# Kernel tuning notes

Measured on AMD Instinct MI355X. Metric: run time of the kernel, lower is better.

## Reference

```python
import jax, jax.numpy as jnp
import numpy as np

D_MODEL = 1024
N_HEADS = 16
D_K = D_MODEL // N_HEADS
ROPE_THETA = 10000.0


def setup_inputs() -> dict:
    key = jax.random.key(0)
    ks = jax.random.split(key, 5)
    B, S = 2, 2048
    std = (2.0 / (D_MODEL + D_MODEL)) ** 0.5
    x = jax.random.normal(ks[0], (B, S, D_MODEL), dtype=jnp.float32)
    Wq = jax.random.normal(ks[1], (D_MODEL, D_MODEL), dtype=jnp.float32) * std
    Wk = jax.random.normal(ks[2], (D_MODEL, D_MODEL), dtype=jnp.float32) * std
    Wv = jax.random.normal(ks[3], (D_MODEL, D_MODEL), dtype=jnp.float32) * std
    Wo = jax.random.normal(ks[4], (D_MODEL, D_MODEL), dtype=jnp.float32) * std
    token_positions = jnp.arange(S, dtype=jnp.int64 if jax.config.jax_enable_x64 else jnp.int32)
    return {"x": x, "Wq": Wq, "Wk": Wk, "Wv": Wv, "Wo": Wo,
            "token_positions": token_positions}


def _apply_rope(t, token_positions):
    # t: [B, H, S, d_k]; token_positions: [S]
    inv_freq = 1.0 / (ROPE_THETA ** (jnp.arange(0, D_K, 2, dtype=jnp.float32) / D_K))  # [d_k/2]
    freqs = token_positions.astype(jnp.float32)[:, None] * inv_freq[None, :]  # [S, d_k/2]
    cos, sin = jnp.cos(freqs), jnp.sin(freqs)
    x1, x2 = t[..., ::2], t[..., 1::2]
    xr = x1 * cos - x2 * sin
    yr = x1 * sin + x2 * cos
    # interleave back to even/odd positions
    out = jnp.stack([xr, yr], axis=-1).reshape(t.shape)
    return out


def reference(x, Wq, Wk, Wv, Wo, token_positions):
    B, S, D = x.shape
    H, dk = N_HEADS, D_K
    # projections: weight is [d_out, d_in], applied as x @ W.T
    def proj_heads(W):
        y = jnp.einsum('bsd,ed->bse', x, W)
        return y.reshape(B, S, H, dk).transpose(0, 2, 1, 3)  # [B,H,S,dk]
    q = proj_heads(Wq)
    k = proj_heads(Wk)
    v = proj_heads(Wv)
    q = _apply_rope(q, token_positions)
    k = _apply_rope(k, token_positions)
    scores = jnp.einsum('bhqd,bhkd->bhqk', q, k) / jnp.sqrt(jnp.float32(dk))
    causal = jnp.tril(jnp.ones((S, S), dtype=bool))
    scores = jnp.where(causal, scores, -jnp.inf)
    attn = jax.nn.softmax(scores, axis=-1)
    out = jnp.einsum('bhqk,bhkd->bhqd', attn, v)  # [B,H,S,dk]
    out = out.transpose(0, 2, 1, 3).reshape(B, S, D)
    return jnp.einsum('bsd,ed->bse', out, Wo)
```

## Files before the change

### kernel.cpp

```cpp
#include <hip/hip_runtime.h>

typedef __bf16 bf16x8 __attribute__((ext_vector_type(8)));
typedef float f32x4 __attribute__((ext_vector_type(4)));
typedef unsigned short u16x8 __attribute__((ext_vector_type(8)));


__device__ __forceinline__ unsigned short f2bf(float f) {
  unsigned u = __builtin_bit_cast(unsigned, f);
  u = (u + 0x7FFFu + ((u >> 16) & 1u)) >> 16;
  return (unsigned short)u;
}

__device__ __forceinline__ unsigned cvt_pk_bf16(float lo, float hi) {
  unsigned r;
  asm("v_cvt_pk_bf16_f32 %0, %1, %2" : "=v"(r) : "v"(lo), "v"(hi));
  return r;
}

__device__ __forceinline__ void load_lds16(const void* g, void* l) {
  __builtin_amdgcn_global_load_lds(
      (__attribute__((address_space(1))) void*)g,
      (__attribute__((address_space(3))) void*)l, 16, 0, 0);
}

__global__ __launch_bounds__(256) void k_convert(
    const float* __restrict__ x,
    const float* __restrict__ wq, const float* __restrict__ wk,
    const float* __restrict__ wv, const float* __restrict__ wo,
    unsigned short* __restrict__ xb,
    unsigned short* __restrict__ wqb, unsigned short* __restrict__ wkb,
    unsigned short* __restrict__ wvb, unsigned short* __restrict__ wob) {
  const int g = blockIdx.x * 256 + threadIdx.x;
  const float* src;
  unsigned short* dst;
  int off;
  if (g < (1 << 20)) {
    src = x; dst = xb; off = g;
  } else {
    const int q = g - (1 << 20);
    const int t = q >> 18;
    off = q & ((1 << 18) - 1);
    src = (t == 0) ? wq : (t == 1) ? wk : (t == 2) ? wv : wo;
    dst = (t == 0) ? wqb : (t == 1) ? wkb : (t == 2) ? wvb : wob;
  }
  const float4 v = ((const float4*)src)[off];
  ushort4 r;
  r.x = f2bf(v.x); r.y = f2bf(v.y); r.z = f2bf(v.z); r.w = f2bf(v.w);
  ((ushort4*)dst)[off] = r;
}

__global__ __launch_bounds__(256) void k_rope_tab(const int* __restrict__ tpos,
                                                  float* __restrict__ ct,
                                                  float* __restrict__ st) {
  const int idx = blockIdx.x * 256 + threadIdx.x;
  const int s = idx >> 5, i = idx & 31;
  const double p = (double)tpos[s];
  const double f = p * pow(10000.0, -(double)(2 * i) / 64.0);
  ct[idx] = (float)cos(f);
  st[idx] = (float)sin(f);
}

__device__ __forceinline__ void gemm_core_1024(
    const unsigned short* __restrict__ Ag,
    const unsigned short* __restrict__ Bg,
    unsigned short* As, unsigned short* Bs, f32x4 (&acc)[4][4], int tid) {
  const int lane = tid & 63;
  const int w = tid >> 6;
  const int wm = (w >> 1) * 64;
  const int wn = (w & 1) * 64;
  const int lr = lane & 15;
  const int lg8 = (lane >> 4) * 8;
  const int c0 = tid, c1 = 256 + tid;
  const int ar0 = c0 >> 2, ac0 = (c0 & 3) * 8;
  const int ar1 = c1 >> 2, ac1 = (c1 & 3) * 8;

  auto stage = [&](int buf, int kt) {
    unsigned short* Ab = As + buf * 4096;
    unsigned short* Bb = Bs + buf * 4096;
    load_lds16(Ag + ar0 * 1024 + kt + ac0, Ab + c0 * 8);
    load_lds16(Ag + ar1 * 1024 + kt + ac1, Ab + c1 * 8);
    load_lds16(Bg + ar0 * 1024 + kt + ac0, Bb + c0 * 8);
    load_lds16(Bg + ar1 * 1024 + kt + ac1, Bb + c1 * 8);
  };

  stage(0, 0);
  stage(1, 32);
  int cur = 0;
  for (int ki = 0; ki < 32; ++ki) {
    if (ki + 2 < 32) {
      int nb = cur + 2; if (nb >= 3) nb -= 3;
      stage(nb, (ki + 2) * 32);
      asm volatile("s_waitcnt vmcnt(8)" ::: "memory");
    } else if (ki + 1 < 32) {
      asm volatile("s_waitcnt vmcnt(4)" ::: "memory");
    } else {
      asm volatile("s_waitcnt vmcnt(0)" ::: "memory");
    }
    __builtin_amdgcn_s_barrier();
    const unsigned short* Ab = As + cur * 4096;
    const unsigned short* Bb = Bs + cur * 4096;
    bf16x8 af[4], bfv[4];
#pragma unroll
    for (int mi = 0; mi < 4; ++mi)
      af[mi] = *(const bf16x8*)(Ab + (wm + mi * 16 + lr) * 32 + lg8);
#pragma unroll
    for (int ni = 0; ni < 4; ++ni)
      bfv[ni] = *(const bf16x8*)(Bb + (wn + ni * 16 + lr) * 32 + lg8);
    __builtin_amdgcn_s_setprio(1);
#pragma unroll
    for (int mi = 0; mi < 4; ++mi)
#pragma unroll
      for (int ni = 0; ni < 4; ++ni)
        acc[mi][ni] = __builtin_amdgcn_mfma_f32_16x16x32_bf16(
            af[mi], bfv[ni], acc[mi][ni], 0, 0, 0);
    __builtin_amdgcn_s_setprio(0);
    __builtin_amdgcn_s_barrier();
    ++cur; if (cur == 3) cur = 0;
  }
}

__global__ __launch_bounds__(256) void k_proj(
    const unsigned short* __restrict__ Xb,
    const unsigned short* __restrict__ Wq, const unsigned short* __restrict__ Wk,
    const unsigned short* __restrict__ Wv,
    const float* __restrict__ ctab, const float* __restrict__ stab,
    unsigned short* __restrict__ Qo, unsigned short* __restrict__ Ko,
    unsigned short* __restrict__ Vo) {
  __shared__ __align__(16) unsigned short As[3 * 128 * 32];
  __shared__ __align__(16) unsigned short Bs[3 * 128 * 32];
  const int z = blockIdx.z;
  const unsigned short* Wsel = (z == 0) ? Wq : (z == 1) ? Wk : Wv;
  unsigned short* Out = (z == 0) ? Qo : (z == 1) ? Ko : Vo;
  const int tid = threadIdx.x;
  const int bm = blockIdx.x * 128, bn = blockIdx.y * 128;
  f32x4 acc[4][4] = {};
  gemm_core_1024(Xb + (size_t)bm * 1024, Wsel + (size_t)bn * 1024, As, Bs, acc, tid);

  const int lane = tid & 63, w = tid >> 6;
  const int wm = (w >> 1) * 64, wn = (w & 1) * 64;
  const int lr = lane & 15, lg = lane >> 4;

  if (z == 2) {
#pragma unroll
    for (int mi = 0; mi < 4; ++mi) {
      const int r0 = bm + wm + mi * 16 + lg * 4;
      const int s = r0 & 2047, b = r0 >> 11;
#pragma unroll
      for (int ni = 0; ni < 4; ++ni) {
        const int e = bn + wn + ni * 16 + lr;
        const int h = e >> 6, d = e & 63;
        ushort4 pk;
        pk.x = f2bf(acc[mi][ni][0]);
        pk.y = f2bf(acc[mi][ni][1]);
        pk.z = f2bf(acc[mi][ni][2]);
        pk.w = f2bf(acc[mi][ni][3]);
        *(ushort4*)&Out[((size_t)(b * 16 + h) * 64 + d) * 2048 + s] = pk;
      }
    }
    return;
  }

  const bool odd = lane & 1;
#pragma unroll
  for (int mi = 0; mi < 4; ++mi) {
#pragma unroll
    for (int ni = 0; ni < 4; ++ni) {
#pragma unroll
      for (int reg = 0; reg < 4; ++reg) {
        const int r = bm + wm + mi * 16 + lg * 4 + reg;
        const int e = bn + wn + ni * 16 + lr;
        float val = acc[mi][ni][reg];
        const float partner = __shfl_xor(val, 1);
        const int s = r & 2047, b = r >> 11;
        const int h = e >> 6, d = e & 63;
        const int i = d >> 1;
        const float c = ctab[s * 32 + i];
        const float sn = stab[s * 32 + i];
        const float outv = odd ? (val * c + partner * sn) : (val * c - partner * sn);
        Out[((size_t)(b * 16 + h) * 2048 + s) * 64 + d] = f2bf(outv);
      }
    }
  }
}

__global__ __launch_bounds__(64, 2) void k_attn(
    const unsigned short* __restrict__ Q, const unsigned short* __restrict__ K,
    const unsigned short* __restrict__ Vt, unsigned short* __restrict__ O) {
  __shared__ __align__(16) unsigned short Vs[2][64 * 64];
  __shared__ __align__(16) unsigned short Pl[16 * 68];
  const int L = blockIdx.x;
  const int bh = (L & 7) * 4 + ((L >> 3) & 3);
  const int p = L >> 5;
  const int qrowA = p * 16, qrowB = (127 - p) * 16;
  const int Ta = (qrowA + 79) >> 6;
  const int Tb = (qrowB + 79) >> 6;
  const int lane = threadIdx.x & 63;
  const int lr = lane & 15, lg = lane >> 4;
  const unsigned short* Qg = Q + (size_t)bh * 2048 * 64;
  const unsigned short* Kg = K + (size_t)bh * 2048 * 64;
  const unsigned short* Vg = Vt + (size_t)bh * 64 * 2048;

  bf16x8 qfA[2], qfB[2];
#pragma unroll
  for (int h = 0; h < 2; ++h) {
    qfA[h] = *(const bf16x8*)(Qg + (qrowA + lr) * 64 + h * 32 + lg * 8);
    qfB[h] = *(const bf16x8*)(Qg + (qrowB + lr) * 64 + h * 32 + lg * 8);
  }

  f32x4 oA[4] = {}, oB[4] = {};
  float mA = -__builtin_inff(), lA = 0.f;
  float mB = -__builtin_inff(), lB = 0.f;

  const float SCL = 0.125f * 1.44269504088896f;

  const int kbase = lr * 64 + lg * 8;
  const int vbase = (lane >> 3) * 2048 + (((lane & 7) ^ (lane >> 3)) * 8);

  auto loadK = [&](bf16x8 (&kd)[4][2], int kv) {
    const unsigned short* base = Kg + (size_t)kv * 4096 + kbase;
#pragma unroll
    for (int nt = 0; nt < 4; ++nt)
#pragma unroll
      for (int h = 0; h < 2; ++h)
        kd[nt][h] = *(const bf16x8*)(base + nt * 1024 + h * 32);
  };
  auto issueV = [&](int buf, int kv) {
    const unsigned short* src = Vg + kv * 64 + vbase;
    unsigned short* dst = &Vs[buf][0] + lane * 8;
#pragma unroll
    for (int i0 = 0; i0 < 8; ++i0)
      load_lds16(src + i0 * 16384, dst + i0 * 512);
  };

  auto process = [&](f32x4 (&s)[4], float& m, float& l, f32x4 (&oacc)[4],
                     int qrow, bool needmask, int kv) {
    if (needmask) {
      const int qg = qrow + lr;
#pragma unroll
      for (int nt = 0; nt < 4; ++nt)
#pragma unroll
        for (int reg = 0; reg < 4; ++reg) {
          const int kg = kv * 64 + nt * 16 + lg * 4 + reg;
          if (kg > qg) s[nt][reg] = -__builtin_inff();
        }
    }
    float t0 = fmaxf(fmaxf(s[0][0], s[0][1]), fmaxf(s[0][2], s[0][3]));
    float t1 = fmaxf(fmaxf(s[1][0], s[1][1]), fmaxf(s[1][2], s[1][3]));
    float t2 = fmaxf(fmaxf(s[2][0], s[2][1]), fmaxf(s[2][2], s[2][3]));
    float t3 = fmaxf(fmaxf(s[3][0], s[3][1]), fmaxf(s[3][2], s[3][3]));
    float pm = fmaxf(fmaxf(t0, t1), fmaxf(t2, t3));
    pm = fmaxf(pm, __shfl_xor(pm, 16));
    pm = fmaxf(pm, __shfl_xor(pm, 32));
    if (__any(pm > m)) {
      const float mn = fmaxf(m, pm);
      const float al = exp2f(SCL * (m - mn));
      m = mn;
      l *= al;
#pragma unroll
      for (int nt = 0; nt < 4; ++nt)
#pragma unroll
        for (int reg = 0; reg < 4; ++reg) oacc[nt][reg] *= al;
    }
    const float msc = SCL * m;
    float rs = 0.f;
    unsigned short* prow = Pl + lr * 68;
#pragma unroll
    for (int nt = 0; nt < 4; ++nt) {
      const float p0 = exp2f(s[nt][0] * SCL - msc);
      const float p1 = exp2f(s[nt][1] * SCL - msc);
      const float p2 = exp2f(s[nt][2] * SCL - msc);
      const float p3 = exp2f(s[nt][3] * SCL - msc);
      rs += (p0 + p1) + (p2 + p3);
      const unsigned w01 = cvt_pk_bf16(p0, p1);
      const unsigned w23 = cvt_pk_bf16(p2, p3);
      ushort4 pk;
      pk.x = (unsigned short)w01; pk.y = (unsigned short)(w01 >> 16);
      pk.z = (unsigned short)w23; pk.w = (unsigned short)(w23 >> 16);
      *(ushort4*)(prow + nt * 16 + lg * 4) = pk;
    }
    rs += __shfl_xor(rs, 16);
    rs += __shfl_xor(rs, 32);
    l += rs;
  };

  bf16x8 kbufA[4][2], kbufB[4][2];
  loadK(kbufA, 0);
  issueV(0, 0);

  auto iter = [&](int t, bf16x8 (&kc)[4][2], bf16x8 (&kn)[4][2]) {
    const bool more = (t + 1 < Tb);
    const bool actA = (t < Ta);
    asm volatile("s_waitcnt lgkmcnt(0)" ::: "memory");
    if (more) { loadK(kn, t + 1); issueV((t + 1) & 1, t + 1); }

    f32x4 sB[4], sA[4];
    __builtin_amdgcn_s_setprio(1);
#pragma unroll
    for (int nt = 0; nt < 4; ++nt) {
      f32x4 z = {0.f, 0.f, 0.f, 0.f};
      z = __builtin_amdgcn_mfma_f32_16x16x32_bf16(kc[nt][0], qfB[0], z, 0, 0, 0);
      sB[nt] = __builtin_amdgcn_mfma_f32_16x16x32_bf16(kc[nt][1], qfB[1], z, 0, 0, 0);
    }
    if (actA)
#pragma unroll
      for (int nt = 0; nt < 4; ++nt) {
        f32x4 z = {0.f, 0.f, 0.f, 0.f};
        z = __builtin_amdgcn_mfma_f32_16x16x32_bf16(kc[nt][0], qfA[0], z, 0, 0, 0);
        sA[nt] = __builtin_amdgcn_mfma_f32_16x16x32_bf16(kc[nt][1], qfA[1], z, 0, 0, 0);
      }
    __builtin_amdgcn_s_setprio(0);

    process(sB, mB, lB, oB, qrowB, t == Tb - 1, t);
    bf16x8 paB[2], paA[2];
#pragma unroll
    for (int ks = 0; ks < 2; ++ks)
      paB[ks] = *(const bf16x8*)(Pl + lr * 68 + ks * 32 + lg * 8);
    if (actA) {
      process(sA, mA, lA, oA, qrowA, t == Ta - 1, t);
#pragma unroll
      for (int ks = 0; ks < 2; ++ks)
        paA[ks] = *(const bf16x8*)(Pl + lr * 68 + ks * 32 + lg * 8);
    }

    if (more) asm volatile("s_waitcnt vmcnt(16)" ::: "memory");
    else      asm volatile("s_waitcnt vmcnt(0)" ::: "memory");

    const unsigned short* Vw = &Vs[t & 1][0];
    __builtin_amdgcn_s_setprio(1);
#pragma unroll
    for (int nt = 0; nt < 4; ++nt) {
      const int row = nt * 16 + lr;
      const bf16x8 vb0 = *(const bf16x8*)(Vw + row * 64 + ((lg ^ (row & 7)) * 8));
      const bf16x8 vb1 = *(const bf16x8*)(Vw + row * 64 + (((lg + 4) ^ (row & 7)) * 8));
      oB[nt] = __builtin_amdgcn_mfma_f32_16x16x32_bf16(vb0, paB[0], oB[nt], 0, 0, 0);
      oB[nt] = __builtin_amdgcn_mfma_f32_16x16x32_bf16(vb1, paB[1], oB[nt], 0, 0, 0);
      if (actA) {
        oA[nt] = __builtin_amdgcn_mfma_f32_16x16x32_bf16(vb0, paA[0], oA[nt], 0, 0, 0);
        oA[nt] = __builtin_amdgcn_mfma_f32_16x16x32_bf16(vb1, paA[1], oA[nt], 0, 0, 0);
      }
    }
    __builtin_amdgcn_s_setprio(0);
  };

  int t = 0;
  for (;;) {
    iter(t, kbufA, kbufB); ++t; if (t >= Tb) break;
    iter(t, kbufB, kbufA); ++t; if (t >= Tb) break;
  }

  const int b = bh >> 4, h = bh & 15;
  auto wrO = [&](f32x4 (&oacc)[4], float l, int qrow) {
    const float inv = 1.0f / l;
    unsigned short* dst = &O[((size_t)b * 2048 + qrow + lr) * 1024 + h * 64];
#pragma unroll
    for (int nt = 0; nt < 4; ++nt) {
      const unsigned w01 = cvt_pk_bf16(oacc[nt][0] * inv, oacc[nt][1] * inv);
      const unsigned w23 = cvt_pk_bf16(oacc[nt][2] * inv, oacc[nt][3] * inv);
      ushort4 pk;
      pk.x = (unsigned short)w01; pk.y = (unsigned short)(w01 >> 16);
      pk.z = (unsigned short)w23; pk.w = (unsigned short)(w23 >> 16);
      *(ushort4*)(dst + nt * 16 + lg * 4) = pk;
    }
  };
  wrO(oA, lA, qrowA);
  wrO(oB, lB, qrowB);
}

__global__ __launch_bounds__(256) void k_out(const unsigned short* __restrict__ Ab,
                                             const unsigned short* __restrict__ Wo,
                                             float* __restrict__ Out) {
  __shared__ __align__(16) unsigned short As[3 * 128 * 32];
  __shared__ __align__(16) unsigned short Bs[3 * 128 * 32];
  const int tid = threadIdx.x;
  const int bm = blockIdx.x * 128, bn = blockIdx.y * 128;
  f32x4 acc[4][4] = {};
  gemm_core_1024(Ab + (size_t)bm * 1024, Wo + (size_t)bn * 1024, As, Bs, acc, tid);
  const int lane = tid & 63, w = tid >> 6;
  const int wm = (w >> 1) * 64, wn = (w & 1) * 64;
  const int lr = lane & 15, lg = lane >> 4;
#pragma unroll
  for (int mi = 0; mi < 4; ++mi)
#pragma unroll
    for (int ni = 0; ni < 4; ++ni)
#pragma unroll
      for (int reg = 0; reg < 4; ++reg) {
        const int r = bm + wm + mi * 16 + lg * 4 + reg;
        const int e = bn + wn + ni * 16 + lr;
        Out[(size_t)r * 1024 + e] = acc[mi][ni][reg];
      }
}

extern "C" void kernel_launch(void* const* d_in, const int* in_sizes, int n_in,
                              void* d_out, int out_size, void* d_ws, size_t ws_size,
                              hipStream_t stream) {
  const float* x = (const float*)d_in[0];
  const float* Wq = (const float*)d_in[1];
  const float* Wk = (const float*)d_in[2];
  const float* Wv = (const float*)d_in[3];
  const float* Wo = (const float*)d_in[4];
  const int* tpos = (const int*)d_in[5];
  float* out = (float*)d_out;
  char* ws = (char*)d_ws;
  const size_t MB = 1024 * 1024;
  unsigned short* xb = (unsigned short*)(ws);
  unsigned short* wqb = (unsigned short*)(ws + 8 * MB);
  unsigned short* wkb = (unsigned short*)(ws + 10 * MB);
  unsigned short* wvb = (unsigned short*)(ws + 12 * MB);
  unsigned short* wob = (unsigned short*)(ws + 14 * MB);
  unsigned short* Qb = (unsigned short*)(ws + 16 * MB);
  unsigned short* Kb = (unsigned short*)(ws + 24 * MB);
  unsigned short* Vtb = (unsigned short*)(ws + 32 * MB);
  unsigned short* Ab = (unsigned short*)(ws + 40 * MB);
  float* ctab = (float*)(ws + 48 * MB);
  float* stab = (float*)(ws + 48 * MB + 256 * 1024);

  k_convert<<<dim3(8192), dim3(256), 0, stream>>>(x, Wq, Wk, Wv, Wo, xb, wqb, wkb,
                                                  wvb, wob);
  k_rope_tab<<<dim3(256), dim3(256), 0, stream>>>(tpos, ctab, stab);
  k_proj<<<dim3(32, 8, 3), dim3(256), 0, stream>>>(xb, wqb, wkb, wvb, ctab, stab,
                                                   Qb, Kb, Vtb);
  k_attn<<<dim3(2048), dim3(64), 0, stream>>>(Qb, Kb, Vtb, Ab);
  k_out<<<dim3(32, 8), dim3(256), 0, stream>>>(Ab, wob, out);
}
```

Measured before the change: 156.2 us.

## Load V fragments directly to registers, compute softmax row sums by MFMA, shrink out-proj tile

The attention kernel drops the LDS staging of V and instead double-buffers V fragments in registers straight from global memory, along with K. It gives each query group its own P buffer in LDS. Softmax row sums are now computed with an MFMA against a ones vector instead of shuffle reductions. The output projection switches to 64-row tiles so it launches twice as many blocks. The changes aim to cut LDS traffic, waits and shuffles, and to improve occupancy, at the cost of more VGPRs and less coalesced V loads.

New measurement: 205.9 us. 1.32x slower.

```diff
diff --git a/kernel.cpp b/kernel.cpp
--- a/kernel.cpp
+++ b/kernel.cpp
@@ -119,6 +119,63 @@
   }
 }
 
+__device__ __forceinline__ void gemm_core_bm64(
+    const unsigned short* __restrict__ Ag,
+    const unsigned short* __restrict__ Bg,
+    unsigned short* As, unsigned short* Bs, f32x4 (&acc)[2][4], int tid) {
+  const int lane = tid & 63;
+  const int w = tid >> 6;
+  const int wm = (w >> 1) * 32;
+  const int wn = (w & 1) * 64;
+  const int lr = lane & 15;
+  const int lg8 = (lane >> 4) * 8;
+  const int ar = tid >> 2, ac = (tid & 3) * 8;
+  const int c0 = tid, c1 = 256 + tid;
+  const int br0 = c0 >> 2, bc0 = (c0 & 3) * 8;
+  const int br1 = c1 >> 2, bc1 = (c1 & 3) * 8;
+
+  auto stage = [&](int buf, int kt) {
+    load_lds16(Ag + ar * 1024 + kt + ac, As + buf * 2048 + tid * 8);
+    load_lds16(Bg + br0 * 1024 + kt + bc0, Bs + buf * 4096 + c0 * 8);
+    load_lds16(Bg + br1 * 1024 + kt + bc1, Bs + buf * 4096 + c1 * 8);
+  };
+
+  stage(0, 0);
+  stage(1, 32);
+  int cur = 0;
+  for (int ki = 0; ki < 32; ++ki) {
+    if (ki + 2 < 32) {
+      int nb = cur + 2; if (nb >= 3) nb -= 3;
+      stage(nb, (ki + 2) * 32);
+      asm volatile("s_waitcnt vmcnt(6)" ::: "memory");
+    } else if (ki + 1 < 32) {
+      asm volatile("s_waitcnt vmcnt(3)" ::: "memory");
+    } else {
+      asm volatile("s_waitcnt vmcnt(0)" ::: "memory");
+    }
+    __builtin_amdgcn_s_barrier();
+    const unsigned short* Ab = As + cur * 2048;
+    const unsigned short* Bb = Bs + cur * 4096;
+    bf16x8 af[2], bfv[4];
+#pragma unroll
+    for (int mi = 0; mi < 2; ++mi)
+      af[mi] = *(const bf16x8*)(Ab + (wm + mi * 16 + lr) * 32 + lg8);
+#pragma unroll
+    for (int ni = 0; ni < 4; ++ni)
+      bfv[ni] = *(const bf16x8*)(Bb + (wn + ni * 16 + lr) * 32 + lg8);
+    __builtin_amdgcn_s_setprio(1);
+#pragma unroll
+    for (int mi = 0; mi < 2; ++mi)
+#pragma unroll
+      for (int ni = 0; ni < 4; ++ni)
+        acc[mi][ni] = __builtin_amdgcn_mfma_f32_16x16x32_bf16(
+            af[mi], bfv[ni], acc[mi][ni], 0, 0, 0);
+    __builtin_amdgcn_s_setprio(0);
+    __builtin_amdgcn_s_barrier();
+    ++cur; if (cur == 3) cur = 0;
+  }
+}
+
 __global__ __launch_bounds__(256) void k_proj(
     const unsigned short* __restrict__ Xb,
     const unsigned short* __restrict__ Wq, const unsigned short* __restrict__ Wk,
@@ -186,8 +243,8 @@
 __global__ __launch_bounds__(64, 2) void k_attn(
     const unsigned short* __restrict__ Q, const unsigned short* __restrict__ K,
     const unsigned short* __restrict__ Vt, unsigned short* __restrict__ O) {
-  __shared__ __align__(16) unsigned short Vs[2][64 * 64];
-  __shared__ __align__(16) unsigned short Pl[16 * 68];
+  __shared__ __align__(16) unsigned short PlB[16 * 68];
+  __shared__ __align__(16) unsigned short PlA[16 * 68];
   const int L = blockIdx.x;
   const int bh = (L & 7) * 4 + ((L >> 3) & 3);
   const int p = L >> 5;
@@ -207,14 +264,19 @@
     qfB[h] = *(const bf16x8*)(Qg + (qrowB + lr) * 64 + h * 32 + lg * 8);
   }
 
+  u16x8 ouv;
+#pragma unroll
+  for (int j = 0; j < 8; ++j) ouv[j] = 0x3F80;
+  const bf16x8 onesf = __builtin_bit_cast(bf16x8, ouv);
+
   f32x4 oA[4] = {}, oB[4] = {};
-  float mA = -__builtin_inff(), lA = 0.f;
-  float mB = -__builtin_inff(), lB = 0.f;
+  f32x4 lAa = {}, lBa = {};
+  float mA = -__builtin_inff(), mB = -__builtin_inff();
 
   const float SCL = 0.125f * 1.44269504088896f;
 
   const int kbase = lr * 64 + lg * 8;
-  const int vbase = (lane >> 3) * 2048 + (((lane & 7) ^ (lane >> 3)) * 8);
+  const int vbase = lr * 2048 + lg * 8;
 
   auto loadK = [&](bf16x8 (&kd)[4][2], int kv) {
     const unsigned short* base = Kg + (size_t)kv * 4096 + kbase;
@@ -224,16 +286,17 @@
       for (int h = 0; h < 2; ++h)
         kd[nt][h] = *(const bf16x8*)(base + nt * 1024 + h * 32);
   };
-  auto issueV = [&](int buf, int kv) {
-    const unsigned short* src = Vg + kv * 64 + vbase;
-    unsigned short* dst = &Vs[buf][0] + lane * 8;
-#pragma unroll
-    for (int i0 = 0; i0 < 8; ++i0)
-      load_lds16(src + i0 * 16384, dst + i0 * 512);
-  };
-
-  auto process = [&](f32x4 (&s)[4], float& m, float& l, f32x4 (&oacc)[4],
-                     int qrow, bool needmask, int kv) {
+  auto loadV = [&](bf16x8 (&vd)[4][2], int kv) {
+    const unsigned short* base = Vg + vbase + kv * 64;
+#pragma unroll
+    for (int nt = 0; nt < 4; ++nt)
+#pragma unroll
+      for (int ks = 0; ks < 2; ++ks)
+        vd[nt][ks] = *(const bf16x8*)(base + nt * 16 * 2048 + ks * 32);
+  };
+
+  auto soft = [&](f32x4 (&s)[4], float& m, f32x4& la, f32x4 (&oacc)[4],
+                  int qrow, bool needmask, int kv, unsigned short* Pl) {
     if (needmask) {
       const int qg = qrow + lr;
 #pragma unroll
@@ -255,14 +318,14 @@
       const float mn = fmaxf(m, pm);
       const float al = exp2f(SCL * (m - mn));
       m = mn;
-      l *= al;
+#pragma unroll
+      for (int reg = 0; reg < 4; ++reg) la[reg] *= al;
 #pragma unroll
       for (int nt = 0; nt < 4; ++nt)
 #pragma unroll
         for (int reg = 0; reg < 4; ++reg) oacc[nt][reg] *= al;
     }
     const float msc = SCL * m;
-    float rs = 0.f;
     unsigned short* prow = Pl + lr * 68;
 #pragma unroll
     for (int nt = 0; nt < 4; ++nt) {
@@ -270,7 +333,6 @@
       const float p1 = exp2f(s[nt][1] * SCL - msc);
       const float p2 = exp2f(s[nt][2] * SCL - msc);
       const float p3 = exp2f(s[nt][3] * SCL - msc);
-      rs += (p0 + p1) + (p2 + p3);
       const unsigned w01 = cvt_pk_bf16(p0, p1);
       const unsigned w23 = cvt_pk_bf16(p2, p3);
       ushort4 pk;
@@ -278,20 +340,17 @@
       pk.z = (unsigned short)w23; pk.w = (unsigned short)(w23 >> 16);
       *(ushort4*)(prow + nt * 16 + lg * 4) = pk;
     }
-    rs += __shfl_xor(rs, 16);
-    rs += __shfl_xor(rs, 32);
-    l += rs;
-  };
-
-  bf16x8 kbufA[4][2], kbufB[4][2];
+  };
+
+  bf16x8 kbufA[4][2], kbufB[4][2], vbufA[4][2], vbufB[4][2];
   loadK(kbufA, 0);
-  issueV(0, 0);
-
-  auto iter = [&](int t, bf16x8 (&kc)[4][2], bf16x8 (&kn)[4][2]) {
+  loadV(vbufA, 0);
+
+  auto iter = [&](int t, bf16x8 (&kc)[4][2], bf16x8 (&kn)[4][2],
+                  bf16x8 (&vc)[4][2], bf16x8 (&vn)[4][2]) {
     const bool more = (t + 1 < Tb);
     const bool actA = (t < Ta);
-    asm volatile("s_waitcnt lgkmcnt(0)" ::: "memory");
-    if (more) { loadK(kn, t + 1); issueV((t + 1) & 1, t + 1); }
+    if (more) { loadK(kn, t + 1); loadV(vn, t + 1); }
 
     f32x4 sB[4], sA[4];
     __builtin_amdgcn_s_setprio(1);
@@ -310,33 +369,36 @@
       }
     __builtin_amdgcn_s_setprio(0);
 
-    process(sB, mB, lB, oB, qrowB, t == Tb - 1, t);
     bf16x8 paB[2], paA[2];
-#pragma unroll
-    for (int ks = 0; ks < 2; ++ks)
-      paB[ks] = *(const bf16x8*)(Pl + lr * 68 + ks * 32 + lg * 8);
     if (actA) {
-      process(sA, mA, lA, oA, qrowA, t == Ta - 1, t);
+      soft(sB, mB, lBa, oB, qrowB, t == Tb - 1, t, PlB);
+      soft(sA, mA, lAa, oA, qrowA, t == Ta - 1, t, PlA);
+#pragma unroll
+      for (int ks = 0; ks < 2; ++ks) {
+        paB[ks] = *(const bf16x8*)(PlB + lr * 68 + ks * 32 + lg * 8);
+        paA[ks] = *(const bf16x8*)(PlA + lr * 68 + ks * 32 + lg * 8);
+      }
+    } else {
+      soft(sB, mB, lBa, oB, qrowB, t == Tb - 1, t, PlB);
 #pragma unroll
       for (int ks = 0; ks < 2; ++ks)
-        paA[ks] = *(const bf16x8*)(Pl + lr * 68 + ks * 32 + lg * 8);
-    }
-
-    if (more) asm volatile("s_waitcnt vmcnt(16)" ::: "memory");
-    else      asm volatile("s_waitcnt vmcnt(0)" ::: "memory");
-
-    const unsigned short* Vw = &Vs[t & 1][0];
+        paB[ks] = *(const bf16x8*)(PlB + lr * 68 + ks * 32 + lg * 8);
+    }
+
     __builtin_amdgcn_s_setprio(1);
+    lBa = __builtin_amdgcn_mfma_f32_16x16x32_bf16(onesf, paB[0], lBa, 0, 0, 0);
+    lBa = __builtin_amdgcn_mfma_f32_16x16x32_bf16(onesf, paB[1], lBa, 0, 0, 0);
+    if (actA) {
+      lAa = __builtin_amdgcn_mfma_f32_16x16x32_bf16(onesf, paA[0], lAa, 0, 0, 0);
+      lAa = __builtin_amdgcn_mfma_f32_16x16x32_bf16(onesf, paA[1], lAa, 0, 0, 0);
+    }
 #pragma unroll
     for (int nt = 0; nt < 4; ++nt) {
-      const int row = nt * 16 + lr;
-      const bf16x8 vb0 = *(const bf16x8*)(Vw + row * 64 + ((lg ^ (row & 7)) * 8));
-      const bf16x8 vb1 = *(const bf16x8*)(Vw + row * 64 + (((lg + 4) ^ (row & 7)) * 8));
-      oB[nt] = __builtin_amdgcn_mfma_f32_16x16x32_bf16(vb0, paB[0], oB[nt], 0, 0, 0);
-      oB[nt] = __builtin_amdgcn_mfma_f32_16x16x32_bf16(vb1, paB[1], oB[nt], 0, 0, 0);
+      oB[nt] = __builtin_amdgcn_mfma_f32_16x16x32_bf16(vc[nt][0], paB[0], oB[nt], 0, 0, 0);
+      oB[nt] = __builtin_amdgcn_mfma_f32_16x16x32_bf16(vc[nt][1], paB[1], oB[nt], 0, 0, 0);
       if (actA) {
-        oA[nt] = __builtin_amdgcn_mfma_f32_16x16x32_bf16(vb0, paA[0], oA[nt], 0, 0, 0);
-        oA[nt] = __builtin_amdgcn_mfma_f32_16x16x32_bf16(vb1, paA[1], oA[nt], 0, 0, 0);
+        oA[nt] = __builtin_amdgcn_mfma_f32_16x16x32_bf16(vc[nt][0], paA[0], oA[nt], 0, 0, 0);
+        oA[nt] = __builtin_amdgcn_mfma_f32_16x16x32_bf16(vc[nt][1], paA[1], oA[nt], 0, 0, 0);
       }
     }
     __builtin_amdgcn_s_setprio(0);
@@ -344,8 +406,8 @@
 
   int t = 0;
   for (;;) {
-    iter(t, kbufA, kbufB); ++t; if (t >= Tb) break;
-    iter(t, kbufB, kbufA); ++t; if (t >= Tb) break;
+    iter(t, kbufA, kbufB, vbufA, vbufB); ++t; if (t >= Tb) break;
+    iter(t, kbufB, kbufA, vbufB, vbufA); ++t; if (t >= Tb) break;
   }
 
   const int b = bh >> 4, h = bh & 15;
@@ -362,24 +424,24 @@
       *(ushort4*)(dst + nt * 16 + lg * 4) = pk;
     }
   };
-  wrO(oA, lA, qrowA);
-  wrO(oB, lB, qrowB);
+  wrO(oA, lAa[0], qrowA);
+  wrO(oB, lBa[0], qrowB);
 }
 
 __global__ __launch_bounds__(256) void k_out(const unsigned short* __restrict__ Ab,
                                              const unsigned short* __restrict__ Wo,
                                              float* __restrict__ Out) {
-  __shared__ __align__(16) unsigned short As[3 * 128 * 32];
+  __shared__ __align__(16) unsigned short As[3 * 64 * 32];
   __shared__ __align__(16) unsigned short Bs[3 * 128 * 32];
   const int tid = threadIdx.x;
-  const int bm = blockIdx.x * 128, bn = blockIdx.y * 128;
-  f32x4 acc[4][4] = {};
-  gemm_core_1024(Ab + (size_t)bm * 1024, Wo + (size_t)bn * 1024, As, Bs, acc, tid);
+  const int bm = blockIdx.x * 64, bn = blockIdx.y * 128;
+  f32x4 acc[2][4] = {};
+  gemm_core_bm64(Ab + (size_t)bm * 1024, Wo + (size_t)bn * 1024, As, Bs, acc, tid);
   const int lane = tid & 63, w = tid >> 6;
-  const int wm = (w >> 1) * 64, wn = (w & 1) * 64;
+  const int wm = (w >> 1) * 32, wn = (w & 1) * 64;
   const int lr = lane & 15, lg = lane >> 4;
 #pragma unroll
-  for (int mi = 0; mi < 4; ++mi)
+  for (int mi = 0; mi < 2; ++mi)
 #pragma unroll
     for (int ni = 0; ni < 4; ++ni)
 #pragma unroll
@@ -420,5 +482,5 @@
   k_proj<<<dim3(32, 8, 3), dim3(256), 0, stream>>>(xb, wqb, wkb, wvb, ctab, stab,
                                                    Qb, Kb, Vtb);
   k_attn<<<dim3(2048), dim3(64), 0, stream>>>(Qb, Kb, Vtb, Ab);
-  k_out<<<dim3(32, 8), dim3(256), 0, stream>>>(Ab, wob, out);
-}
+  k_out<<<dim3(64, 8), dim3(256), 0, stream>>>(Ab, wob, out);
+}
```
